# Performance work log

Hardware: AMD Instinct MI355X
Metric: run time of the kernel (lower is better)

The kernel has to match this reference:

```python
import jax, jax.numpy as jnp
import numpy as np

LAMDA = 0.5
TEMPERATURE = 0.07
EPS = 1e-5


def setup_inputs() -> dict:
    key = jax.random.key(0)
    k1, k2, k3 = jax.random.split(key, 3)
    N, D = 8192, 128
    features = jax.random.normal(k1, (N, D), dtype=jnp.float32)
    labels = jax.random.randint(k2, (N,), 0, 100, dtype=jnp.int64 if jax.config.jax_enable_x64 else jnp.int32)
    domain_labels = jax.random.randint(k3, (N,), 0, 4, dtype=jnp.int64 if jax.config.jax_enable_x64 else jnp.int32)
    return {"features": features, "labels": labels, "domain_labels": domain_labels}


def reference(features, labels, domain_labels):
    N = features.shape[0]
    # L2-normalize rows (torch.nn.functional.normalize, eps=1e-12)
    norms = jnp.maximum(jnp.linalg.norm(features, axis=1, keepdims=True), 1e-12)
    f = features / norms
    sim = jnp.matmul(f, f.T) / TEMPERATURE  # [N, N]

    same_label = labels[:, None] == labels[None, :]
    same_dom = domain_labels[:, None] == domain_labels[None, :]
    offdiag = ~jnp.eye(N, dtype=bool)

    # per-pair domain weight: lamda in-domain, (1-lamda) out-of-domain
    w_exp = jnp.where(same_dom, LAMDA, 1.0 - LAMDA) * jnp.exp(sim)

    # denominator: all off-diagonal pairs (positives + negatives), weighted
    denom = jnp.sum(jnp.where(offdiag, w_exp, 0.0), axis=1) + EPS  # [N]

    pos = same_label & offdiag
    log_frac = jnp.log(w_exp / denom[:, None] + EPS)
    num_pos = jnp.sum(pos, axis=1)  # [N]
    loss_i = jnp.sum(jnp.where(pos, log_frac, 0.0), axis=1) / jnp.maximum(num_pos, 1)

    # anchors with zero positives produce NaN in torch and are skipped
    valid = num_pos > 0
    nans = jnp.sum(~valid)
    loss = -jnp.sum(jnp.where(valid, loss_i, 0.0))
    return loss / (N - nans + 1)
```

## Files before the change

kernel.cpp:

```cpp
#include <hip/hip_runtime.h>

#define NROWS 8192
#define DDIM  128
#define NBLK  (NROWS / 128)
#define NLAB  100
#define GCAP  160
#define GNJT  (GCAP / 16)
#define EPSV  1e-5f
#define LN2F  0.69314718055994530942f
#define FSCALE 4.53981643f

typedef short s16x8 __attribute__((ext_vector_type(8)));
typedef float f32x4 __attribute__((ext_vector_type(4)));
typedef unsigned short u16;
typedef unsigned int u32;

__device__ __forceinline__ u16 f2bf(float x) {
  u32 b = __builtin_bit_cast(u32, x);
  u32 r = (b + 0x7FFFu + ((b >> 16) & 1u)) >> 16;
  return (u16)r;
}

__global__ __launch_bounds__(256) void zero_kernel(
    float* __restrict__ denom, float* __restrict__ Lsum) {
  denom[blockIdx.x * 256 + threadIdx.x] = 0.0f;
  if (blockIdx.x == 0 && threadIdx.x == 0) *Lsum = 0.0f;
}

__global__ __launch_bounds__(256) void norm_kernel(
    const float* __restrict__ feat, u16* __restrict__ g) {
  int wave = threadIdx.x >> 6;
  int lane = threadIdx.x & 63;
  int row = (blockIdx.x << 2) + wave;
  const float* fr = feat + (size_t)row * DDIM + (lane << 1);
  float2 v = *(const float2*)fr;
  float ss = v.x * v.x + v.y * v.y;
#pragma unroll
  for (int m = 1; m < 64; m <<= 1) ss += __shfl_xor(ss, m);
  float inv = FSCALE / fmaxf(sqrtf(ss), 1e-12f);
  ushort2 o;
  o.x = f2bf(v.x * inv);
  o.y = f2bf(v.y * inv);
  *(ushort2*)(g + (size_t)row * DDIM + (lane << 1)) = o;
}

__global__ __launch_bounds__(256) void bucket_kernel(
    const int* __restrict__ lab, int* __restrict__ offs,
    int* __restrict__ cnts, int* __restrict__ rowlist) {
  __shared__ int h[NLAB], cur[NLAB], off[NLAB];
  int tid = threadIdx.x;
  if (tid < NLAB) h[tid] = 0;
  __syncthreads();
  for (int i = tid; i < NROWS; i += 256) atomicAdd(&h[lab[i]], 1);
  __syncthreads();
  if (tid == 0) {
    int s = 0;
    for (int l = 0; l < NLAB; ++l) { off[l] = s; s += h[l]; }
  }
  __syncthreads();
  if (tid < NLAB) { cur[tid] = off[tid]; offs[tid] = off[tid]; cnts[tid] = h[tid]; }
  __syncthreads();
  for (int i = tid; i < NROWS; i += 256) {
    int p = atomicAdd(&cur[lab[i]], 1);
    rowlist[p] = i;
  }
}

#define LOADB_TO(bv, BsArr, jt)                                              \
  _Pragma("unroll")                                                          \
  for (int kc = 0; kc < 4; ++kc) {                                           \
    const int c_ = (kc << 2) + lh;                                           \
    bv[kc] = *(const s16x8*)(&BsArr[(size_t)((jt)*16 + lr) * DDIM +          \
                                    ((c_ ^ (lr & 7)) << 3)]);                \
  }

#define MFMA_TO(accv, bv, init0, init1)                                      \
  accv[0] = init0; accv[1] = init1;                                          \
  __builtin_amdgcn_s_setprio(1);                                             \
  _Pragma("unroll")                                                          \
  for (int kc = 0; kc < 4; ++kc) {                                           \
    accv[0] = __builtin_amdgcn_mfma_f32_16x16x32_bf16(a[0][kc], bv[kc],      \
                                                      accv[0], 0, 0, 0);     \
    accv[1] = __builtin_amdgcn_mfma_f32_16x16x32_bf16(a[1][kc], bv[kc],      \
                                                      accv[1], 0, 0, 0);     \
  }                                                                          \
  __builtin_amdgcn_s_setprio(0);

#define EPI_T(accv, jt)                                                      \
  {                                                                          \
    const int tj0 = j0 + (jt)*16;                                            \
    float csum = 0.f;                                                        \
    if (diagblk) {                                                           \
      _Pragma("unroll")                                                      \
      for (int rf = 0; rf < 2; ++rf)                                         \
      _Pragma("unroll")                                                      \
        for (int r = 0; r < 4; ++r) {                                        \
          float e_ = __builtin_amdgcn_exp2f(accv[rf][r]);                    \
          e_ = (gibase[rf] + r == tj0 + lr) ? 0.0f : e_;                     \
          dacc[rf][r] += e_;                                                 \
        }                                                                    \
    } else {                                                                 \
      _Pragma("unroll")                                                      \
      for (int rf = 0; rf < 2; ++rf)                                         \
      _Pragma("unroll")                                                      \
        for (int r = 0; r < 4; ++r) {                                        \
          float e_ = __builtin_amdgcn_exp2f(accv[rf][r]);                    \
          dacc[rf][r] += e_;                                                 \
          csum += e_;                                                        \
        }                                                                    \
      csum += __shfl_xor(csum, 16);                                          \
      csum += __shfl_xor(csum, 32);                                          \
      ccol[jt] = csum;                                                       \
    }                                                                        \
  }

__global__ __launch_bounds__(256, 4) void denom_tri(
    const u16* __restrict__ g, float* __restrict__ denom) {
  const int bi = blockIdx.x, bj = blockIdx.y;
  if (bj < bi) return;
  __shared__ u16 Bs[128 * DDIM];
  const int tid = threadIdx.x;
  const int wave = tid >> 6, lane = tid & 63;
  const int lr = lane & 15, lh = lane >> 4;
  const int i0 = bi * 128 + wave * 32;
  const int j0 = bj * 128;
  const bool diagblk = (bi == bj);

  {
    const int cs = (tid & 15) ^ ((tid >> 4) & 7);
#pragma unroll
    for (int k = 0; k < 8; ++k) {
      const u16* src = g + (size_t)(j0 + k * 16 + (tid >> 4)) * DDIM + (cs << 3);
      u16* dst = &Bs[(size_t)(k * 16 + (wave << 2)) * DDIM];
      __builtin_amdgcn_global_load_lds(
          (const __attribute__((address_space(1))) void*)src,
          (__attribute__((address_space(3))) void*)dst, 16, 0, 0);
    }
  }

  s16x8 a[2][4];
#pragma unroll
  for (int rf = 0; rf < 2; ++rf) {
    const u16* gr = g + (size_t)(i0 + rf * 16 + lr) * DDIM + lh * 8;
#pragma unroll
    for (int kc = 0; kc < 4; ++kc) a[rf][kc] = *(const s16x8*)(gr + kc * 32);
  }
  const int gibase[2] = {i0 + lh * 4, i0 + 16 + lh * 4};

  asm volatile("s_waitcnt vmcnt(0)" ::: "memory");
  __builtin_amdgcn_s_barrier();

  float dacc[2][4] = {};
  float ccol[8] = {};
  const f32x4 m1 = f32x4{-1.f, -1.f, -1.f, -1.f};

  s16x8 b0[4], b1[4];
  f32x4 acc0[2], acc1[2];

  LOADB_TO(b0, Bs, 0)
  MFMA_TO(acc0, b0, m1, m1)
#pragma unroll
  for (int p = 0; p < 3; ++p) {
    LOADB_TO(b1, Bs, 2 * p + 1)
    MFMA_TO(acc1, b1, m1, m1)
    EPI_T(acc0, 2 * p)
    LOADB_TO(b0, Bs, 2 * p + 2)
    MFMA_TO(acc0, b0, m1, m1)
    EPI_T(acc1, 2 * p + 1)
  }
  LOADB_TO(b1, Bs, 7)
  MFMA_TO(acc1, b1, m1, m1)
  EPI_T(acc0, 6)
  EPI_T(acc1, 7)

#pragma unroll
  for (int rf = 0; rf < 2; ++rf)
#pragma unroll
    for (int r = 0; r < 4; ++r) {
      float v = dacc[rf][r];
      v += __shfl_xor(v, 1); v += __shfl_xor(v, 2);
      v += __shfl_xor(v, 4); v += __shfl_xor(v, 8);
      if (lr == 0) atomicAdd(&denom[gibase[rf] + r], v);
    }
  if (!diagblk) {
#pragma unroll
    for (int jt = 0; jt < 8; ++jt)
      if (lane < 16) atomicAdd(&denom[j0 + jt * 16 + lane], ccol[jt]);
  }
}

__global__ __launch_bounds__(320) void group_loss(
    const u16* __restrict__ g, const int* __restrict__ offs,
    const int* __restrict__ cnts, const int* __restrict__ rowlist,
    const float* __restrict__ denom, float* __restrict__ Lsum) {
  __shared__ u16 Bs[GCAP * DDIM];
  const int lb = blockIdx.x;
  const int cnt = cnts[lb];
  if (cnt < 2) return;
  const int off = offs[lb];
  const int tid = threadIdx.x;
  const int wave = tid >> 6, lane = tid & 63;
  const int lr = lane & 15, lh = lane >> 4;

#pragma unroll
  for (int s = 0; s < 8; ++s) {
    const int m = s * 320 + tid;
    const int rloc = m >> 4, cc = m & 15;
    const int cs = cc ^ (rloc & 7);
    const int grow = rowlist[off + (rloc < cnt ? rloc : 0)];
    const u16* src = g + (size_t)grow * DDIM + (cs << 3);
    u16* dst = &Bs[(size_t)(s * 320 + wave * 64) * 8];
    __builtin_amdgcn_global_load_lds(
        (const __attribute__((address_space(1))) void*)src,
        (__attribute__((address_space(3))) void*)dst, 16, 0, 0);
  }

  s16x8 a[2][4];
#pragma unroll
  for (int rf = 0; rf < 2; ++rf) {
    const int ar = wave * 32 + rf * 16 + lr;
    const int gar = rowlist[off + (ar < cnt ? ar : 0)];
    const u16* gr = g + (size_t)gar * DDIM + lh * 8;
#pragma unroll
    for (int kc = 0; kc < 4; ++kc) a[rf][kc] = *(const s16x8*)(gr + kc * 32);
  }
  const int erow[2] = {wave * 32 + lh * 4, wave * 32 + 16 + lh * 4};
  f32x4 cinit[2];
#pragma unroll
  for (int rf = 0; rf < 2; ++rf)
#pragma unroll
    for (int r = 0; r < 4; ++r) {
      const int er = erow[rf] + r;
      const int gi = rowlist[off + (er < cnt ? er : 0)];
      cinit[rf][r] = -__builtin_amdgcn_logf(denom[gi] + EPSV) - 1.0f;
    }

  asm volatile("s_waitcnt vmcnt(0)" ::: "memory");
  __builtin_amdgcn_s_barrier();

  float lacc[2][4] = {};

#pragma unroll
  for (int jt = 0; jt < GNJT; ++jt) {
    s16x8 b[4];
    LOADB_TO(b, Bs, jt)
    f32x4 acc[2];
    MFMA_TO(acc, b, cinit[0], cinit[1])
    const int col = jt * 16 + lr;
    const bool colok = (col < cnt);
#pragma unroll
    for (int rf = 0; rf < 2; ++rf)
#pragma unroll
      for (int r = 0; r < 4; ++r) {
        const int er = erow[rf] + r;
        const bool valid = colok && (er < cnt) && (er != col);
        float x = __builtin_amdgcn_exp2f(acc[rf][r]) + EPSV;
        float lf = __builtin_amdgcn_logf(x);
        lacc[rf][r] += valid ? lf : 0.0f;
      }
  }

  const float scale = LN2F / (float)(cnt - 1);
  float wtot = 0.f;
#pragma unroll
  for (int rf = 0; rf < 2; ++rf)
#pragma unroll
    for (int r = 0; r < 4; ++r) {
      float v = lacc[rf][r];
      v += __shfl_xor(v, 1); v += __shfl_xor(v, 2);
      v += __shfl_xor(v, 4); v += __shfl_xor(v, 8);
      const int er = erow[rf] + r;
      if (lr == 0 && er < cnt) wtot += v * scale;
    }
  wtot += __shfl_xor(wtot, 1);  wtot += __shfl_xor(wtot, 2);
  wtot += __shfl_xor(wtot, 4);  wtot += __shfl_xor(wtot, 8);
  wtot += __shfl_xor(wtot, 16); wtot += __shfl_xor(wtot, 32);
  if (lane == 0 && wtot != 0.0f) atomicAdd(Lsum, wtot);
}

__global__ __launch_bounds__(64) void final_kernel(
    const int* __restrict__ cnts, const float* __restrict__ Lsum,
    float* __restrict__ out) {
  int lane = threadIdx.x;
  int v = 0;
  if (lane < NLAB) { int c = cnts[lane]; v += (c > 1) ? c : 0; }
  if (lane + 64 < NLAB) { int c = cnts[lane + 64]; v += (c > 1) ? c : 0; }
  v += __shfl_xor(v, 1);  v += __shfl_xor(v, 2);
  v += __shfl_xor(v, 4);  v += __shfl_xor(v, 8);
  v += __shfl_xor(v, 16); v += __shfl_xor(v, 32);
  if (lane == 0) out[0] = -Lsum[0] / (float)(v + 1);
}

extern "C" void kernel_launch(void* const* d_in, const int* in_sizes, int n_in,
                              void* d_out, int out_size, void* d_ws, size_t ws_size,
                              hipStream_t stream) {
  const float* feat = (const float*)d_in[0];
  const int* labels = (const int*)d_in[1];
  float* out = (float*)d_out;

  char* ws = (char*)d_ws;
  u16* g        = (u16*)(ws);
  float* denom  = (float*)(ws + (2u << 20));
  int* offs     = (int*)(ws + (2u << 20) + 32768);
  int* cnts     = (int*)(ws + (2u << 20) + 33280);
  float* Lsum   = (float*)(ws + (2u << 20) + 33792);
  int* rowlist  = (int*)(ws + (2u << 20) + 65536);

  zero_kernel<<<NROWS / 256, 256, 0, stream>>>(denom, Lsum);
  norm_kernel<<<NROWS / 4, 256, 0, stream>>>(feat, g);
  bucket_kernel<<<1, 256, 0, stream>>>(labels, offs, cnts, rowlist);
  denom_tri<<<dim3(NBLK, NBLK), 256, 0, stream>>>(g, denom);
  group_loss<<<NLAB, 320, 0, stream>>>(g, offs, cnts, rowlist, denom, Lsum);
  final_kernel<<<1, 64, 0, stream>>>(cnts, Lsum, out);
}
```

Baseline: 67.80 us.

## Split group loss column tiles across two blocks and fold zeroing into other kernels

Removes the separate zero kernel: norm_kernel now zeroes denom per row and bucket_kernel zeroes Lsum. bucket_kernel grows to 1024 threads to shorten its serial histogram loops. group_loss is launched with a second grid dimension that splits each label's column tiles between two blocks in an interleaved pattern, halving per-block LDS staging and MFMA work so that 200 blocks run instead of 100. The cost is more atomic contributions to Lsum and duplicated A-row and denominator loads in each split block.

After: 59.94 us. 1.13x faster.

```diff
diff --git a/kernel.cpp b/kernel.cpp
--- a/kernel.cpp
+++ b/kernel.cpp
@@ -5,7 +5,8 @@
 #define NBLK  (NROWS / 128)
 #define NLAB  100
 #define GCAP  160
-#define GNJT  (GCAP / 16)
+#define GSPL  2
+#define GTPB  5
 #define EPSV  1e-5f
 #define LN2F  0.69314718055994530942f
 #define FSCALE 4.53981643f
@@ -21,14 +22,9 @@
   return (u16)r;
 }
 
-__global__ __launch_bounds__(256) void zero_kernel(
-    float* __restrict__ denom, float* __restrict__ Lsum) {
-  denom[blockIdx.x * 256 + threadIdx.x] = 0.0f;
-  if (blockIdx.x == 0 && threadIdx.x == 0) *Lsum = 0.0f;
-}
-
 __global__ __launch_bounds__(256) void norm_kernel(
-    const float* __restrict__ feat, u16* __restrict__ g) {
+    const float* __restrict__ feat, u16* __restrict__ g,
+    float* __restrict__ denom) {
   int wave = threadIdx.x >> 6;
   int lane = threadIdx.x & 63;
   int row = (blockIdx.x << 2) + wave;
@@ -42,16 +38,19 @@
   o.x = f2bf(v.x * inv);
   o.y = f2bf(v.y * inv);
   *(ushort2*)(g + (size_t)row * DDIM + (lane << 1)) = o;
-}
-
-__global__ __launch_bounds__(256) void bucket_kernel(
+  if (lane == 0) denom[row] = 0.0f;
+}
+
+__global__ __launch_bounds__(1024) void bucket_kernel(
     const int* __restrict__ lab, int* __restrict__ offs,
-    int* __restrict__ cnts, int* __restrict__ rowlist) {
+    int* __restrict__ cnts, int* __restrict__ rowlist,
+    float* __restrict__ Lsum) {
   __shared__ int h[NLAB], cur[NLAB], off[NLAB];
   int tid = threadIdx.x;
   if (tid < NLAB) h[tid] = 0;
+  if (tid == 1023) *Lsum = 0.0f;
   __syncthreads();
-  for (int i = tid; i < NROWS; i += 256) atomicAdd(&h[lab[i]], 1);
+  for (int i = tid; i < NROWS; i += 1024) atomicAdd(&h[lab[i]], 1);
   __syncthreads();
   if (tid == 0) {
     int s = 0;
@@ -60,7 +59,7 @@
   __syncthreads();
   if (tid < NLAB) { cur[tid] = off[tid]; offs[tid] = off[tid]; cnts[tid] = h[tid]; }
   __syncthreads();
-  for (int i = tid; i < NROWS; i += 256) {
+  for (int i = tid; i < NROWS; i += 1024) {
     int p = atomicAdd(&cur[lab[i]], 1);
     rowlist[p] = i;
   }
@@ -193,21 +192,25 @@
     const u16* __restrict__ g, const int* __restrict__ offs,
     const int* __restrict__ cnts, const int* __restrict__ rowlist,
     const float* __restrict__ denom, float* __restrict__ Lsum) {
-  __shared__ u16 Bs[GCAP * DDIM];
+  __shared__ u16 Bs[GTPB * 16 * DDIM];
   const int lb = blockIdx.x;
+  const int z = blockIdx.y;
   const int cnt = cnts[lb];
   if (cnt < 2) return;
+  if (z * 16 >= cnt) return;
   const int off = offs[lb];
   const int tid = threadIdx.x;
   const int wave = tid >> 6, lane = tid & 63;
   const int lr = lane & 15, lh = lane >> 4;
 
 #pragma unroll
-  for (int s = 0; s < 8; ++s) {
+  for (int s = 0; s < 4; ++s) {
     const int m = s * 320 + tid;
     const int rloc = m >> 4, cc = m & 15;
+    const int jt_l = rloc >> 4, rr = rloc & 15;
+    const int gidx = (jt_l * GSPL + z) * 16 + rr;
     const int cs = cc ^ (rloc & 7);
-    const int grow = rowlist[off + (rloc < cnt ? rloc : 0)];
+    const int grow = rowlist[off + (gidx < cnt ? gidx : 0)];
     const u16* src = g + (size_t)grow * DDIM + (cs << 3);
     u16* dst = &Bs[(size_t)(s * 320 + wave * 64) * 8];
     __builtin_amdgcn_global_load_lds(
@@ -241,12 +244,12 @@
   float lacc[2][4] = {};
 
 #pragma unroll
-  for (int jt = 0; jt < GNJT; ++jt) {
+  for (int jt = 0; jt < GTPB; ++jt) {
     s16x8 b[4];
     LOADB_TO(b, Bs, jt)
     f32x4 acc[2];
     MFMA_TO(acc, b, cinit[0], cinit[1])
-    const int col = jt * 16 + lr;
+    const int col = (jt * GSPL + z) * 16 + lr;
     const bool colok = (col < cnt);
 #pragma unroll
     for (int rf = 0; rf < 2; ++rf)
@@ -306,10 +309,9 @@
   float* Lsum   = (float*)(ws + (2u << 20) + 33792);
   int* rowlist  = (int*)(ws + (2u << 20) + 65536);
 
-  zero_kernel<<<NROWS / 256, 256, 0, stream>>>(denom, Lsum);
-  norm_kernel<<<NROWS / 4, 256, 0, stream>>>(feat, g);
-  bucket_kernel<<<1, 256, 0, stream>>>(labels, offs, cnts, rowlist);
+  norm_kernel<<<NROWS / 4, 256, 0, stream>>>(feat, g, denom);
+  bucket_kernel<<<1, 1024, 0, stream>>>(labels, offs, cnts, rowlist, Lsum);
   denom_tri<<<dim3(NBLK, NBLK), 256, 0, stream>>>(g, denom);
-  group_loss<<<NLAB, 320, 0, stream>>>(g, offs, cnts, rowlist, denom, Lsum);
+  group_loss<<<dim3(NLAB, GSPL), 320, 0, stream>>>(g, offs, cnts, rowlist, denom, Lsum);
   final_kernel<<<1, 64, 0, stream>>>(cnts, Lsum, out);
 }
```
